# Optimization experiments

Measured on AMD Instinct MI355X. Metric: run time of the kernel, lower is better.

Reference implementation:

```python
import jax, jax.numpy as jnp
import numpy as np

BATCH, INPUT_DIM, HIDDEN_DIM, SEQ_LENGTH = 128, 256, 512, 1024


def setup_inputs() -> dict:
    key = jax.random.key(0)
    k1, k2, k3, k4, k5 = jax.random.split(key, 5)
    s = 1.0 / np.sqrt(HIDDEN_DIM)  # PyTorch GRU init: U(-1/sqrt(H), 1/sqrt(H))
    return {
        "input_features": jax.random.normal(k1, (BATCH, INPUT_DIM), dtype=jnp.float32),
        # PyTorch layout: rows stacked as [reset; update; new], each [H, *]
        "w_ih": jax.random.uniform(k2, (3 * HIDDEN_DIM, INPUT_DIM), minval=-s, maxval=s, dtype=jnp.float32),
        "w_hh": jax.random.uniform(k3, (3 * HIDDEN_DIM, HIDDEN_DIM), minval=-s, maxval=s, dtype=jnp.float32),
        "b_ih": jax.random.uniform(k4, (3 * HIDDEN_DIM,), minval=-s, maxval=s, dtype=jnp.float32),
        "b_hh": jax.random.uniform(k5, (3 * HIDDEN_DIM,), minval=-s, maxval=s, dtype=jnp.float32),
    }


def reference(input_features, w_ih, w_hh, b_ih, b_hh):
    # Decoder: run the GRU cell SEQ_LENGTH times with the SAME input x each
    # step, feeding back the hidden state; collect per-step outputs.
    B = input_features.shape[0]
    H = w_hh.shape[1]
    # Input contribution is constant across steps -> compute once.  [B, 3H]
    gi = input_features @ w_ih.T + b_ih
    gi_r, gi_z, gi_n = jnp.split(gi, 3, axis=-1)

    def step(h, _):
        gh = h @ w_hh.T + b_hh  # [B, 3H]
        gh_r, gh_z, gh_n = jnp.split(gh, 3, axis=-1)
        r = jax.nn.sigmoid(gi_r + gh_r)
        z = jax.nn.sigmoid(gi_z + gh_z)
        n = jnp.tanh(gi_n + r * gh_n)
        h_new = (1.0 - z) * n + z * h
        return h_new, h_new

    h0 = jnp.zeros((B, H), dtype=input_features.dtype)
    _, outs = jax.lax.scan(step, h0, None, length=SEQ_LENGTH)  # [S, B, H]
    return jnp.transpose(outs, (1, 0, 2))  # [B, SEQ_LENGTH, H]
```

## Files before the change

kernel.cpp:

```cpp
#include <hip/hip_runtime.h>
#include <hip/hip_bf16.h>
#include <stdint.h>


constexpr int SEQ = 1024;
constexpr int BATCH = 128;
constexpr int IND = 256;
constexpr int HD = 512;
constexpr int BG = 8;
constexpr int HG = 32;
constexpr int ROWS = BATCH / BG;
constexpr int NT = 3;

using frag16 = __attribute__((ext_vector_type(8))) short;
using f32x4  = __attribute__((ext_vector_type(4))) float;

constexpr size_t WS_HBUF  = 0;
constexpr size_t WS_FLAGS = (size_t)2 * BATCH * HD * 2;

__device__ __forceinline__ float sigmoid_f(float x) {
    return 1.f / (1.f + __expf(-x));
}
__device__ __forceinline__ float tanh_f(float x) {
    float e = __expf(2.f * x);
    return 1.f - 2.f / (e + 1.f);
}
__device__ __forceinline__ short f2bf(float x) {
    return (short)__bfloat16_as_ushort(__float2bfloat16(x));
}

__global__ __launch_bounds__(64) void gru_kernel(
    const float* __restrict__ x,
    const float* __restrict__ w_ih,
    const float* __restrict__ w_hh,
    const float* __restrict__ b_ih,
    const float* __restrict__ b_hh,
    unsigned* __restrict__ hbuf_u32,
    unsigned* __restrict__ flags,
    float* __restrict__ out)
{
    const int lane = threadIdx.x;
    const int bg = blockIdx.x & 7;
    const int hg = blockIdx.x >> 3;
    const int b0 = bg * ROWS;
    const int c0 = hg * 16;
    const int nlo = lane & 15;
    const int quad = lane >> 4;

    int gcol[NT];
    gcol[0] = c0 + nlo;
    gcol[1] = HD + c0 + nlo;
    gcol[2] = 2 * HD + c0 + nlo;

    __shared__ frag16 ldsB[NT * 16 * 64];
#pragma unroll
    for (int t = 0; t < NT; ++t) {
        for (int kc = 0; kc < 16; ++kc) {
            const float* src = w_hh + (size_t)gcol[t] * HD + kc * 32 + quad * 8;
            float4 v0 = *(const float4*)src;
            float4 v1 = *(const float4*)(src + 4);
            frag16 f;
            f[0] = f2bf(v0.x); f[1] = f2bf(v0.y); f[2] = f2bf(v0.z); f[3] = f2bf(v0.w);
            f[4] = f2bf(v1.x); f[5] = f2bf(v1.y); f[6] = f2bf(v1.z); f[7] = f2bf(v1.w);
            ldsB[(t * 16 + kc) * 64 + lane] = f;
        }
    }

    float gi[NT][4];
    float bhn = b_hh[gcol[2]];
#pragma unroll
    for (int t = 0; t < NT; ++t) {
        float bi = b_ih[gcol[t]] + ((t < 2) ? b_hh[gcol[t]] : 0.f);
#pragma unroll
        for (int r = 0; r < 4; ++r) gi[t][r] = bi;
    }
    for (int r = 0; r < 4; ++r) {
        const float4* xr = (const float4*)(x + (size_t)(b0 + quad * 4 + r) * IND);
        for (int kc = 0; kc < IND / 4; ++kc) {
            float4 xv = xr[kc];
#pragma unroll
            for (int t = 0; t < NT; ++t) {
                float4 wv = ((const float4*)(w_ih + (size_t)gcol[t] * IND))[kc];
                gi[t][r] += xv.x * wv.x + xv.y * wv.y + xv.z * wv.z + xv.w * wv.w;
            }
        }
    }

    const int HWORDS = BATCH * HD / 2;
    const uint64_t a_dw = ((uint64_t)(b0 + nlo) * HD + quad * 8) >> 1;

    float hreg[4];
#pragma unroll
    for (int r = 0; r < 4; ++r) hreg[r] = 0.f;

    unsigned* myflag = flags + bg * HG + hg;
    unsigned* pollflag = flags + bg * HG + (lane & 31);

    for (int s = 0; s < SEQ; ++s) {
        f32x4 C[NT];
#pragma unroll
        for (int t = 0; t < NT; ++t) C[t] = (f32x4){0.f, 0.f, 0.f, 0.f};

        if (s > 0) {
            unsigned long long* hb =
                (unsigned long long*)(hbuf_u32 + (s & 1) * HWORDS);
            unsigned long long a0[16], a1[16];
#pragma unroll
            for (int kc = 0; kc < 16; ++kc) {
                unsigned long long* p = hb + ((a_dw + kc * 16) >> 1);
                a0[kc] = __hip_atomic_load(p,     __ATOMIC_RELAXED, __HIP_MEMORY_SCOPE_SYSTEM);
                a1[kc] = __hip_atomic_load(p + 1, __ATOMIC_RELAXED, __HIP_MEMORY_SCOPE_SYSTEM);
            }
#pragma unroll
            for (int kc = 0; kc < 16; ++kc) {
                union { unsigned long long u[2]; frag16 f; } af;
                af.u[0] = a0[kc];
                af.u[1] = a1[kc];
#pragma unroll
                for (int t = 0; t < NT; ++t) {
                    frag16 bfr = ldsB[(t * 16 + kc) * 64 + lane];
                    C[t] = __builtin_amdgcn_mfma_f32_16x16x32_bf16(af.f, bfr, C[t], 0, 0, 0);
                }
            }
        }

        unsigned* hw = hbuf_u32 + ((s + 1) & 1) * HWORDS;
#pragma unroll
        for (int r = 0; r < 4; ++r) {
            float gr  = gi[0][r] + C[0][r];
            float gz  = gi[1][r] + C[1][r];
            float ghn = C[2][r] + bhn;
            float rr = sigmoid_f(gr);
            float zz = sigmoid_f(gz);
            float nn = tanh_f(gi[2][r] + rr * ghn);
            float hn = (1.f - zz) * nn + zz * hreg[r];
            hreg[r] = hn;
            int row = b0 + quad * 4 + r;
            int col = c0 + nlo;
            out[(uint64_t)row * (SEQ * HD) + (uint64_t)s * HD + col] = hn;
            unsigned own = (unsigned)(unsigned short)f2bf(hn);
            unsigned other = (unsigned)__shfl_xor((int)own, 1);
            if ((lane & 1) == 0) {
                unsigned dw = own | (other << 16);
                __hip_atomic_store(hw + ((unsigned)(row * HD + col) >> 1), dw,
                                   __ATOMIC_RELAXED, __HIP_MEMORY_SCOPE_SYSTEM);
            }
        }

        if (s < SEQ - 1) {
            asm volatile("s_waitcnt vmcnt(0)" ::: "memory");
            if (lane == 0)
                __hip_atomic_store(myflag, (unsigned)(s + 1),
                                   __ATOMIC_RELAXED, __HIP_MEMORY_SCOPE_SYSTEM);
            bool done = false;
            do {
                unsigned v = __hip_atomic_load(pollflag, __ATOMIC_RELAXED,
                                               __HIP_MEMORY_SCOPE_SYSTEM);
                done = (__ballot(v > (unsigned)s) == ~0ull);
            } while (!done);
            asm volatile("" ::: "memory");
        }
    }
}

extern "C" void kernel_launch(void* const* d_in, const int* in_sizes, int n_in,
                              void* d_out, int out_size, void* d_ws, size_t ws_size,
                              hipStream_t stream) {
    (void)in_sizes; (void)n_in; (void)out_size; (void)ws_size;
    const float* x    = (const float*)d_in[0];
    const float* w_ih = (const float*)d_in[1];
    const float* w_hh = (const float*)d_in[2];
    const float* b_ih = (const float*)d_in[3];
    const float* b_hh = (const float*)d_in[4];

    char* ws = (char*)d_ws;
    unsigned* hbuf  = (unsigned*)(ws + WS_HBUF);
    unsigned* flags = (unsigned*)(ws + WS_FLAGS);

    hipMemsetAsync(flags, 0, (size_t)BG * HG * sizeof(unsigned), stream);
    gru_kernel<<<BG * HG, 64, 0, stream>>>(x, w_ih, w_hh, b_ih, b_hh, hbuf, flags,
                                           (float*)d_out);
}
```

Baseline: 3.358 ms.

## Store hidden-state exchange buffer in fragment-native layout and defer output stores

Rewrites the bf16 hidden-state exchange buffer into a per-batch-group layout that matches the MFMA A-fragment order. Each lane now reads contiguous 16-byte chunks, and writers pack 8 bf16 values via shuffles into two 64-bit stores issued by every eighth lane. The fp32 output stores move after the flag publish, so the s_waitcnt before the flag no longer waits on output traffic. The aim is less exchange latency on the serial per-step critical path, at the cost of extra shuffles.

```diff
diff --git a/kernel.cpp b/kernel.cpp
--- a/kernel.cpp
+++ b/kernel.cpp
@@ -15,8 +15,8 @@
 using frag16 = __attribute__((ext_vector_type(8))) short;
 using f32x4  = __attribute__((ext_vector_type(4))) float;
 
-constexpr size_t WS_HBUF  = 0;
-constexpr size_t WS_FLAGS = (size_t)2 * BATCH * HD * 2;
+constexpr size_t HX_BUF_ULL = (size_t)BG * 2048;
+constexpr size_t WS_FLAGS   = 2 * HX_BUF_ULL * 8;
 
 __device__ __forceinline__ float sigmoid_f(float x) {
     return 1.f / (1.f + __expf(-x));
@@ -25,8 +25,8 @@
     float e = __expf(2.f * x);
     return 1.f - 2.f / (e + 1.f);
 }
-__device__ __forceinline__ short f2bf(float x) {
-    return (short)__bfloat16_as_ushort(__float2bfloat16(x));
+__device__ __forceinline__ unsigned short f2bfu(float x) {
+    return __bfloat16_as_ushort(__float2bfloat16(x));
 }
 
 __global__ __launch_bounds__(64) void gru_kernel(
@@ -35,7 +35,7 @@
     const float* __restrict__ w_hh,
     const float* __restrict__ b_ih,
     const float* __restrict__ b_hh,
-    unsigned* __restrict__ hbuf_u32,
+    unsigned long long* __restrict__ hx,
     unsigned* __restrict__ flags,
     float* __restrict__ out)
 {
@@ -60,8 +60,10 @@
             float4 v0 = *(const float4*)src;
             float4 v1 = *(const float4*)(src + 4);
             frag16 f;
-            f[0] = f2bf(v0.x); f[1] = f2bf(v0.y); f[2] = f2bf(v0.z); f[3] = f2bf(v0.w);
-            f[4] = f2bf(v1.x); f[5] = f2bf(v1.y); f[6] = f2bf(v1.z); f[7] = f2bf(v1.w);
+            f[0] = (short)f2bfu(v0.x); f[1] = (short)f2bfu(v0.y);
+            f[2] = (short)f2bfu(v0.z); f[3] = (short)f2bfu(v0.w);
+            f[4] = (short)f2bfu(v1.x); f[5] = (short)f2bfu(v1.y);
+            f[6] = (short)f2bfu(v1.z); f[7] = (short)f2bfu(v1.w);
             ldsB[(t * 16 + kc) * 64 + lane] = f;
         }
     }
@@ -86,9 +88,6 @@
         }
     }
 
-    const int HWORDS = BATCH * HD / 2;
-    const uint64_t a_dw = ((uint64_t)(b0 + nlo) * HD + quad * 8) >> 1;
-
     float hreg[4];
 #pragma unroll
     for (int r = 0; r < 4; ++r) hreg[r] = 0.f;
@@ -102,14 +101,13 @@
         for (int t = 0; t < NT; ++t) C[t] = (f32x4){0.f, 0.f, 0.f, 0.f};
 
         if (s > 0) {
-            unsigned long long* hb =
-                (unsigned long long*)(hbuf_u32 + (s & 1) * HWORDS);
+            const unsigned long long* hb =
+                hx + ((size_t)(s & 1) * BG + bg) * 2048 + (size_t)lane * 2;
             unsigned long long a0[16], a1[16];
 #pragma unroll
             for (int kc = 0; kc < 16; ++kc) {
-                unsigned long long* p = hb + ((a_dw + kc * 16) >> 1);
-                a0[kc] = __hip_atomic_load(p,     __ATOMIC_RELAXED, __HIP_MEMORY_SCOPE_SYSTEM);
-                a1[kc] = __hip_atomic_load(p + 1, __ATOMIC_RELAXED, __HIP_MEMORY_SCOPE_SYSTEM);
+                a0[kc] = __hip_atomic_load(hb + kc * 128,     __ATOMIC_RELAXED, __HIP_MEMORY_SCOPE_SYSTEM);
+                a1[kc] = __hip_atomic_load(hb + kc * 128 + 1, __ATOMIC_RELAXED, __HIP_MEMORY_SCOPE_SYSTEM);
             }
 #pragma unroll
             for (int kc = 0; kc < 16; ++kc) {
@@ -124,7 +122,8 @@
             }
         }
 
-        unsigned* hw = hbuf_u32 + ((s + 1) & 1) * HWORDS;
+        unsigned long long* hw = hx + ((size_t)((s + 1) & 1) * BG + bg) * 2048;
+        float ov[4];
 #pragma unroll
         for (int r = 0; r < 4; ++r) {
             float gr  = gi[0][r] + C[0][r];
@@ -135,15 +134,18 @@
             float nn = tanh_f(gi[2][r] + rr * ghn);
             float hn = (1.f - zz) * nn + zz * hreg[r];
             hreg[r] = hn;
-            int row = b0 + quad * 4 + r;
-            int col = c0 + nlo;
-            out[(uint64_t)row * (SEQ * HD) + (uint64_t)s * HD + col] = hn;
-            unsigned own = (unsigned)(unsigned short)f2bf(hn);
-            unsigned other = (unsigned)__shfl_xor((int)own, 1);
-            if ((lane & 1) == 0) {
-                unsigned dw = own | (other << 16);
-                __hip_atomic_store(hw + ((unsigned)(row * HD + col) >> 1), dw,
-                                   __ATOMIC_RELAXED, __HIP_MEMORY_SCOPE_SYSTEM);
+            ov[r] = hn;
+            unsigned own = (unsigned)f2bfu(hn);
+            unsigned v0 = own | ((unsigned)__shfl_xor((int)own, 1) << 16);
+            unsigned w1 = (unsigned)__shfl_xor((int)v0, 2);
+            unsigned u2 = (unsigned)__shfl_xor((int)v0, 4);
+            unsigned u3 = (unsigned)__shfl_xor((int)w1, 4);
+            if ((lane & 7) == 0) {
+                unsigned long long lo = (unsigned long long)v0 | ((unsigned long long)w1 << 32);
+                unsigned long long hi = (unsigned long long)u2 | ((unsigned long long)u3 << 32);
+                size_t ci = (size_t)hg * 64 + (size_t)(nlo >> 3) * 32 + (size_t)(quad * 4 + r) * 2;
+                __hip_atomic_store(hw + ci,     lo, __ATOMIC_RELAXED, __HIP_MEMORY_SCOPE_SYSTEM);
+                __hip_atomic_store(hw + ci + 1, hi, __ATOMIC_RELAXED, __HIP_MEMORY_SCOPE_SYSTEM);
             }
         }
 
@@ -152,6 +154,18 @@
             if (lane == 0)
                 __hip_atomic_store(myflag, (unsigned)(s + 1),
                                    __ATOMIC_RELAXED, __HIP_MEMORY_SCOPE_SYSTEM);
+            asm volatile("" ::: "memory");
+        }
+
+        {
+            float* op = out + (size_t)(b0 + quad * 4) * (SEQ * HD) + (size_t)s * HD + c0 + nlo;
+#pragma unroll
+            for (int r = 0; r < 4; ++r)
+                op[(size_t)r * (SEQ * HD)] = ov[r];
+        }
+
+        if (s < SEQ - 1) {
+            asm volatile("" ::: "memory");
             bool done = false;
             do {
                 unsigned v = __hip_atomic_load(pollflag, __ATOMIC_RELAXED,
@@ -174,10 +188,10 @@
     const float* b_hh = (const float*)d_in[4];
 
     char* ws = (char*)d_ws;
-    unsigned* hbuf  = (unsigned*)(ws + WS_HBUF);
+    unsigned long long* hx = (unsigned long long*)ws;
     unsigned* flags = (unsigned*)(ws + WS_FLAGS);
 
     hipMemsetAsync(flags, 0, (size_t)BG * HG * sizeof(unsigned), stream);
-    gru_kernel<<<BG * HG, 64, 0, stream>>>(x, w_ih, w_hh, b_ih, b_hh, hbuf, flags,
+    gru_kernel<<<BG * HG, 64, 0, stream>>>(x, w_ih, w_hh, b_ih, b_hh, hx, flags,
                                            (float*)d_out);
 }
```

Result: slower. 3.461 ms (+3.0%).
